# Performance work log

Hardware: AMD Instinct MI355X
Metric: run time of the kernel (lower is better)

The kernel has to match this reference:

```python
import jax, jax.numpy as jnp
import numpy as np

IN_F, OUT_F = 2048, 2048
N_EXPERTS, RANK, TOP_K = 8, 128, 2


def setup_inputs() -> dict:
    key = jax.random.key(0)
    k_x, k_r, k_a, k_b = jax.random.split(key, 4)
    hidden_states = jax.random.normal(k_x, (4, 4096, IN_F), dtype=jnp.float32)
    # router_proj.weight is [E, in]; we store it transposed so logits = x @ router_w
    router_w = jax.random.normal(k_r, (IN_F, N_EXPERTS), dtype=jnp.float32) * (IN_F ** -0.5)
    # expert e: a_proj [in, rank], b_proj [rank, out] (transposed nn.Linear weights)
    Wa = jax.random.normal(k_a, (N_EXPERTS, IN_F, RANK), dtype=jnp.float32) * (IN_F ** -0.5)
    Wb = jax.random.normal(k_b, (N_EXPERTS, RANK, OUT_F), dtype=jnp.float32) * (RANK ** -0.5)
    return {"hidden_states": hidden_states, "router_w": router_w, "Wa": Wa, "Wb": Wb}


def reference(hidden_states, router_w, Wa, Wb):
    B, S, D = hidden_states.shape
    x = hidden_states.reshape(-1, D)  # [T, in]
    # F.normalize(x, dim=-1): x / max(||x||_2, 1e-12)
    norm = jnp.maximum(jnp.linalg.norm(x, axis=-1, keepdims=True), 1e-12)
    router_logits = (x / norm) @ router_w  # [T, E]
    routing_weights = jax.nn.softmax(router_logits.astype(jnp.float32), axis=-1)
    rw, selected_experts = jax.lax.top_k(routing_weights, TOP_K)  # [T, k]
    rw = rw / jnp.sum(rw, axis=-1, keepdims=True)
    rw = rw.astype(hidden_states.dtype)
    # combine[t, e] = routing weight if expert e selected for token t, else 0.
    combine = jnp.sum(jax.nn.one_hot(selected_experts, N_EXPERTS, dtype=rw.dtype) * rw[..., None], axis=1)  # [T, E]
    out = jnp.zeros((x.shape[0], OUT_F), dtype=hidden_states.dtype)
    for e in range(N_EXPERTS):  # small fixed expert count
        out = out + combine[:, e, None] * ((x @ Wa[e]) @ Wb[e])
    return out.reshape(B, S, OUT_F)
```

## Files before the change

### kernel.cpp

```cpp
#include <hip/hip_runtime.h>
#include <cstdint>
#include <cstddef>

#define TOKENS 16384
#define DIM    2048
#define NEXP   8
#define RANK   128
#define NOUT   2048
#define CAP    8192
#define KSL    8

typedef __attribute__((ext_vector_type(4))) float    f32x4;
typedef __attribute__((ext_vector_type(8))) _Float16 f16x8;
typedef __attribute__((ext_vector_type(4))) _Float16 f16x4;

__device__ __forceinline__ void gload_lds16(const void* g, void* l) {
  __builtin_amdgcn_global_load_lds(
      (const __attribute__((address_space(1))) void*)g,
      (__attribute__((address_space(3))) void*)l, 16, 0, 0);
}

__global__ __launch_bounds__(256) void transpose_cast_f16(
    const float* __restrict__ in, _Float16* __restrict__ out,
    int R, int C, long ostride, long obase)
{
  __shared__ float tile[32][33];
  const int e = blockIdx.z;
  const float* ine = in + (size_t)e * R * C;
  const int c0 = blockIdx.x * 32, r0 = blockIdx.y * 32;
  const int tx = threadIdx.x, ty = threadIdx.y;
#pragma unroll
  for (int j = 0; j < 32; j += 8)
    tile[ty + j][tx] = ine[(size_t)(r0 + ty + j) * C + (c0 + tx)];
  __syncthreads();
#pragma unroll
  for (int j = 0; j < 32; j += 8)
    out[(size_t)e * obase + (size_t)(c0 + ty + j) * ostride + (r0 + tx)] =
        (_Float16)tile[tx][ty + j];
}

__global__ __launch_bounds__(256) void logits_fused_kernel(
    const float* __restrict__ x, const float* __restrict__ rw,
    float* __restrict__ lgpart, float* __restrict__ ssqpart,
    _Float16* __restrict__ xh)
{
  __shared__ __align__(16) char lds[16384];
  char* ldsBh = lds;
  char* ldsBe = lds + 8192;
  const int tid = threadIdx.x;
  const int w = tid >> 6, l = tid & 63;
  const int m0 = blockIdx.x * 128;
  const int ks = blockIdx.y;
  const int kbase = ks * 256;

#pragma unroll
  for (int i = 0; i < 16; ++i) {
    const int idx = tid * 16 + i;
    const int n = idx >> 8, k = idx & 255;
    const float v = (n < 8) ? rw[(size_t)(kbase + k) * 8 + n] : 0.f;
    const _Float16 h = (_Float16)v;
    const _Float16 e = (_Float16)(v - (float)h);
    const int off = n * 512 + ((k * 2) ^ ((n & 7) << 4));
    *(_Float16*)(ldsBh + off) = h;
    *(_Float16*)(ldsBe + off) = e;
  }
  __syncthreads();

  f32x4 acc[2];
  float ssl[2] = {0.f, 0.f};
#pragma unroll
  for (int mf = 0; mf < 2; ++mf)
#pragma unroll
    for (int j = 0; j < 4; ++j) acc[mf][j] = 0.f;

  for (int st = 0; st < 4; ++st) {
#pragma unroll
    for (int kk = 0; kk < 2; ++kk) {
      const int n = l & 15;
      const int bko = n * 512 +
          ((st * 128 + kk * 64 + ((l >> 4) << 4)) ^ ((n & 7) << 4));
      const f16x8 bh = *(const f16x8*)(ldsBh + bko);
      const f16x8 be = *(const f16x8*)(ldsBe + bko);
      const int c = kbase + st * 64 + kk * 32 + ((l >> 4) << 3);
#pragma unroll
      for (int mf = 0; mf < 2; ++mf) {
        const int r = m0 + w * 32 + mf * 16 + (l & 15);
        const float* xp = x + (size_t)r * DIM + c;
        const f32x4 va = *(const f32x4*)(xp);
        const f32x4 vb = *(const f32x4*)(xp + 4);
        float f[8] = {va[0], va[1], va[2], va[3], vb[0], vb[1], vb[2], vb[3]};
        f16x8 ah, ae;
#pragma unroll
        for (int j = 0; j < 8; ++j) {
          ah[j] = (_Float16)f[j];
          ae[j] = (_Float16)(f[j] - (float)ah[j]);
          ssl[mf] = fmaf(f[j], f[j], ssl[mf]);
        }
        *(f16x8*)(xh + (size_t)r * DIM + c) = ah;
        acc[mf] = __builtin_amdgcn_mfma_f32_16x16x32_f16(ae, bh, acc[mf], 0, 0, 0);
        acc[mf] = __builtin_amdgcn_mfma_f32_16x16x32_f16(ah, be, acc[mf], 0, 0, 0);
        acc[mf] = __builtin_amdgcn_mfma_f32_16x16x32_f16(ah, bh, acc[mf], 0, 0, 0);
      }
    }
  }

  const int col = l & 15;
  if (col < 8) {
#pragma unroll
    for (int mf = 0; mf < 2; ++mf) {
      const int rbase = m0 + w * 32 + mf * 16 + ((l >> 4) << 2);
#pragma unroll
      for (int j = 0; j < 4; ++j)
        lgpart[((size_t)ks * TOKENS + rbase + j) * 8 + col] = acc[mf][j];
    }
  }
#pragma unroll
  for (int mf = 0; mf < 2; ++mf) {
    float s = ssl[mf];
    s += __shfl_xor(s, 16, 64);
    s += __shfl_xor(s, 32, 64);
    if (l < 16)
      ssqpart[(size_t)ks * TOKENS + m0 + w * 32 + mf * 16 + l] = s;
  }
}

__global__ __launch_bounds__(256) void softmax_top2_kernel(
    const float* __restrict__ lgpart, const float* __restrict__ ssqpart,
    float* __restrict__ combine, int* __restrict__ pairinfo,
    int* __restrict__ counts, unsigned short* __restrict__ ids16)
{
  const size_t t = (size_t)blockIdx.x * 256 + threadIdx.x;
  float ss = 0.f;
  float lg[8];
#pragma unroll
  for (int e = 0; e < 8; ++e) lg[e] = 0.f;
#pragma unroll
  for (int ks = 0; ks < KSL; ++ks) {
    ss += ssqpart[(size_t)ks * TOKENS + t];
    const float* p = lgpart + ((size_t)ks * TOKENS + t) * 8;
    float4 a = *(const float4*)(p);
    float4 b = *(const float4*)(p + 4);
    lg[0] += a.x; lg[1] += a.y; lg[2] += a.z; lg[3] += a.w;
    lg[4] += b.x; lg[5] += b.y; lg[6] += b.z; lg[7] += b.w;
  }
  const float iv = 1.f / fmaxf(sqrtf(ss), 1e-12f);
#pragma unroll
  for (int e = 0; e < 8; ++e) lg[e] *= iv;
  float b1 = lg[0]; int e1 = 0;
#pragma unroll
  for (int e = 1; e < 8; ++e)
    if (lg[e] > b1) { b1 = lg[e]; e1 = e; }
  float b2 = -3.4e38f; int e2 = 0;
#pragma unroll
  for (int e = 0; e < 8; ++e)
    if (e != e1 && lg[e] > b2) { b2 = lg[e]; e2 = e; }
  const float p2 = expf(b2 - b1);
  const float w1 = 1.f / (1.f + p2);
  const float w2 = p2 * w1;
  float ov[8];
#pragma unroll
  for (int e = 0; e < 8; ++e)
    ov[e] = (e == e1) ? w1 : ((e == e2) ? w2 : 0.f);
  float4* cp = (float4*)(combine + t * 8);
  cp[0] = make_float4(ov[0], ov[1], ov[2], ov[3]);
  cp[1] = make_float4(ov[4], ov[5], ov[6], ov[7]);

  const int a = min(e1, e2), b = max(e1, e2);
  pairinfo[t] = a | (b << 8);
  const int bin = a * 8 + b;
  const int pos = atomicAdd(&counts[bin], 1);
  if (pos < CAP) ids16[bin * CAP + pos] = (unsigned short)t;
}

__global__ void make_items_kernel(const int* __restrict__ counts,
                                  int4* __restrict__ items)
{
  if (threadIdx.x == 0 && blockIdx.x == 0) {
    int j = 0;
    for (int b = 0; b < 64; ++b) {
      int c = counts[b]; if (c > CAP) c = CAP;
      for (int s = 0; s < c; s += 128)
        items[j++] = make_int4(b, b * CAP + s, min(128, c - s), 0);
    }
    for (; j < 192; ++j) items[j] = make_int4(-1, 0, 0, 0);
  }
}

__global__ __launch_bounds__(256) void gemm1_pair_kernel(
    const _Float16* __restrict__ xh, const _Float16* __restrict__ WaT,
    const float* __restrict__ combine, const unsigned short* __restrict__ ids,
    const int4* __restrict__ items, _Float16* __restrict__ Yc)
{
  __shared__ __align__(16) char lds[32768];
  __shared__ int ids_lds[128];
  char* ldsA = lds;
  char* ldsB = lds + 16384;
  const int4 item = items[blockIdx.y];
  if (item.x < 0) return;
  const int slot = blockIdx.x;
  const int e = slot ? (item.x & 7) : (item.x >> 3);
  const int tid = threadIdx.x;
  const int w = tid >> 6, l = tid & 63;
  const int wm = w >> 1, wn = w & 1;

  if (tid < 128)
    ids_lds[tid] = (tid < item.z) ? (int)ids[item.y + tid] : -1;
  __syncthreads();

  const int Lb = w * 1024 + l * 16;
  const _Float16* aptr[4];
  const _Float16* bptr[4];
  int ldst[4];
#pragma unroll
  for (int i = 0; i < 4; ++i) {
    const int L = i * 4096 + Lb;
    const int row = L >> 7;
    const int cb = (L & 127) ^ ((row & 7) << 4);
    int t = ids_lds[row]; if (t < 0) t = 0;
    aptr[i] = xh + (size_t)t * DIM + (cb >> 1);
    bptr[i] = WaT + (size_t)(e * 128 + row) * DIM + (cb >> 1);
    ldst[i] = i * 4096 + w * 1024;
  }

  f32x4 acc[4][4];
#pragma unroll
  for (int p = 0; p < 4; ++p)
#pragma unroll
    for (int q = 0; q < 4; ++q)
#pragma unroll
      for (int j = 0; j < 4; ++j) acc[p][q][j] = 0.f;

  for (int kt = 0; kt < DIM; kt += 64) {
#pragma unroll
    for (int i = 0; i < 4; ++i) {
      gload_lds16(aptr[i] + kt, ldsA + ldst[i]);
      gload_lds16(bptr[i] + kt, ldsB + ldst[i]);
    }
    __syncthreads();
#pragma unroll
    for (int kk = 0; kk < 2; ++kk) {
      const int kb = kk * 64 + ((l >> 4) << 4);
      f16x8 af[4], bfr[4];
#pragma unroll
      for (int mf = 0; mf < 4; ++mf) {
        const int r = (wm << 6) + (mf << 4) + (l & 15);
        af[mf] = *(const f16x8*)(ldsA + r * 128 + (kb ^ ((r & 7) << 4)));
      }
#pragma unroll
      for (int nf = 0; nf < 4; ++nf) {
        const int r = (wn << 6) + (nf << 4) + (l & 15);
        bfr[nf] = *(const f16x8*)(ldsB + r * 128 + (kb ^ ((r & 7) << 4)));
      }
#pragma unroll
      for (int mf = 0; mf < 4; ++mf)
#pragma unroll
        for (int nf = 0; nf < 4; ++nf)
          acc[mf][nf] = __builtin_amdgcn_mfma_f32_16x16x32_f16(
              af[mf], bfr[nf], acc[mf][nf], 0, 0, 0);
    }
    __syncthreads();
  }

  const int cr = (l >> 4) << 2;
  const int cc = l & 15;
#pragma unroll
  for (int mf = 0; mf < 4; ++mf) {
    const int lr0 = (wm << 6) + (mf << 4) + cr;
#pragma unroll
    for (int j = 0; j < 4; ++j) {
      const int t = ids_lds[lr0 + j];
      if (t < 0) continue;
      const float cs = combine[(size_t)t * 8 + e];
      _Float16* yr = Yc + (size_t)t * 256 + slot * 128;
#pragma unroll
      for (int nf = 0; nf < 4; ++nf)
        yr[(wn << 6) + (nf << 4) + cc] = (_Float16)(acc[mf][nf][j] * cs);
    }
  }
}

__global__ __launch_bounds__(256) void gemm2_pair_kernel(
    const _Float16* __restrict__ Y, const _Float16* __restrict__ WbT,
    const unsigned short* __restrict__ ids, const int4* __restrict__ items,
    float* __restrict__ out)
{
  __shared__ __align__(16) char lds[32768];
  __shared__ int ids_lds[128];
  char* ldsA = lds;
  char* ldsB = lds + 16384;
  const int4 item = items[blockIdx.y];
  if (item.x < 0) return;
  const int a = item.x >> 3, b = item.x & 7;
  const int n0 = blockIdx.x * 128;
  const int tid = threadIdx.x;
  const int w = tid >> 6, l = tid & 63;
  const int wm = w >> 1, wn = w & 1;

  if (tid < 128)
    ids_lds[tid] = (tid < item.z) ? (int)ids[item.y + tid] : -1;
  __syncthreads();

  const int Lb = w * 1024 + l * 16;
  const _Float16* aptr[4];
  const _Float16* bptrA[4];
  const _Float16* bptrB[4];
  int ldst[4];
#pragma unroll
  for (int i = 0; i < 4; ++i) {
    const int L = i * 4096 + Lb;
    const int row = L >> 7;
    const int cb = (L & 127) ^ ((row & 7) << 4);
    int t = ids_lds[row]; if (t < 0) t = 0;
    aptr[i]  = Y + (size_t)t * 256 + (cb >> 1);
    bptrA[i] = WbT + (size_t)(n0 + row) * 1024 + a * 128 + (cb >> 1);
    bptrB[i] = WbT + (size_t)(n0 + row) * 1024 + b * 128 + (cb >> 1);
    ldst[i] = i * 4096 + w * 1024;
  }

  f32x4 acc[4][4];
#pragma unroll
  for (int p = 0; p < 4; ++p)
#pragma unroll
    for (int q = 0; q < 4; ++q)
#pragma unroll
      for (int j = 0; j < 4; ++j) acc[p][q][j] = 0.f;

#pragma unroll
  for (int kt = 0; kt < 4; ++kt) {
#pragma unroll
    for (int i = 0; i < 4; ++i) {
      gload_lds16(aptr[i] + kt * 64, ldsA + ldst[i]);
      const _Float16* bs = (kt < 2) ? (bptrA[i] + kt * 64)
                                    : (bptrB[i] + (kt - 2) * 64);
      gload_lds16(bs, ldsB + ldst[i]);
    }
    __syncthreads();
#pragma unroll
    for (int kk = 0; kk < 2; ++kk) {
      const int kb = kk * 64 + ((l >> 4) << 4);
      f16x8 af[4], bfr[4];
#pragma unroll
      for (int mf = 0; mf < 4; ++mf) {
        const int r = (wm << 6) + (mf << 4) + (l & 15);
        af[mf] = *(const f16x8*)(ldsA + r * 128 + (kb ^ ((r & 7) << 4)));
      }
#pragma unroll
      for (int nf = 0; nf < 4; ++nf) {
        const int r = (wn << 6) + (nf << 4) + (l & 15);
        bfr[nf] = *(const f16x8*)(ldsB + r * 128 + (kb ^ ((r & 7) << 4)));
      }
#pragma unroll
      for (int mf = 0; mf < 4; ++mf)
#pragma unroll
        for (int nf = 0; nf < 4; ++nf)
          acc[mf][nf] = __builtin_amdgcn_mfma_f32_16x16x32_f16(
              af[mf], bfr[nf], acc[mf][nf], 0, 0, 0);
    }
    __syncthreads();
  }

  const int cr = (l >> 4) << 2;
  const int cc = l & 15;
#pragma unroll
  for (int mf = 0; mf < 4; ++mf) {
    const int lr0 = (wm << 6) + (mf << 4) + cr;
#pragma unroll
    for (int j = 0; j < 4; ++j) {
      const int t = ids_lds[lr0 + j];
      if (t < 0) continue;
      float* orow = out + (size_t)t * NOUT + n0;
#pragma unroll
      for (int nf = 0; nf < 4; ++nf)
        orow[(wn << 6) + (nf << 4) + cc] = acc[mf][nf][j];
    }
  }
}

extern "C" void kernel_launch(void* const* d_in, const int* in_sizes, int n_in,
                              void* d_out, int out_size, void* d_ws, size_t ws_size,
                              hipStream_t stream) {
  const float* x  = (const float*)d_in[0];
  const float* rw = (const float*)d_in[1];
  const float* Wa = (const float*)d_in[2];
  const float* Wb = (const float*)d_in[3];
  float* out = (float*)d_out;

  char* ws = (char*)d_ws;
  _Float16* xh       = (_Float16*)(ws);
  _Float16* WaT      = (_Float16*)(ws + 67108864);
  _Float16* WbT      = (_Float16*)(ws + 71303168);
  float*    combine  = (float*)   (ws + 75497472);
  int*      pairinfo = (int*)     (ws + 76021760);
  int*      counts   = (int*)     (ws + 76087296);
  int4*     items    = (int4*)    (ws + 76087552);
  unsigned short* ids16 = (unsigned short*)(ws + 76090624);
  _Float16* Yc       = (_Float16*)(ws + 77139200);
  float*    lgpart   = (float*)   (ws + 77139200);
  float*    ssqpart  = (float*)   (ws + 81333504);

  transpose_cast_f16<<<dim3(4, 64, 8), dim3(32, 8), 0, stream>>>(
      Wa, WaT, 2048, 128, 2048, (long)128 * 2048);
  transpose_cast_f16<<<dim3(64, 4, 8), dim3(32, 8), 0, stream>>>(
      Wb, WbT, 128, 2048, 1024, 128);

  logits_fused_kernel<<<dim3(TOKENS / 128, KSL), 256, 0, stream>>>(
      x, rw, lgpart, ssqpart, xh);

  hipMemsetAsync(counts, 0, 64 * sizeof(int), stream);
  softmax_top2_kernel<<<TOKENS / 256, 256, 0, stream>>>(
      lgpart, ssqpart, combine, pairinfo, counts, ids16);
  make_items_kernel<<<1, 64, 0, stream>>>(counts, items);

  gemm1_pair_kernel<<<dim3(2, 192), 256, 0, stream>>>(
      xh, WaT, combine, ids16, items, Yc);
  gemm2_pair_kernel<<<dim3(NOUT / 128, 192), 256, 0, stream>>>(
      Yc, WbT, ids16, items, out);
}
```

Measured before the change: 219.0 us.

## Fuse router logits and top-2 into one kernel; compute both experts per gemm1 block

Replaces the split-K MFMA logits kernel and the separate softmax/top-2 kernel with a single router kernel. Each wave handles one token row at a time, doing fp32 FMA dot products against an LDS-transposed router matrix and reducing with shuffles. This removes the partial-sum buffers and one launch, and it changes routing precision from split-fp16 MFMA to plain fp32. gemm1 now loads the A tile once and computes both paired experts in one block with a 256-wide N tile. That halves A traffic but doubles accumulator registers and raises LDS use to 48KB, which may reduce occupancy.

```diff
diff --git a/kernel.cpp b/kernel.cpp
--- a/kernel.cpp
+++ b/kernel.cpp
@@ -8,7 +8,6 @@
 #define RANK   128
 #define NOUT   2048
 #define CAP    8192
-#define KSL    8
 
 typedef __attribute__((ext_vector_type(4))) float    f32x4;
 typedef __attribute__((ext_vector_type(8))) _Float16 f16x8;
@@ -39,137 +38,92 @@
         (_Float16)tile[tx][ty + j];
 }
 
-__global__ __launch_bounds__(256) void logits_fused_kernel(
+__global__ __launch_bounds__(512) void router_kernel(
     const float* __restrict__ x, const float* __restrict__ rw,
-    float* __restrict__ lgpart, float* __restrict__ ssqpart,
-    _Float16* __restrict__ xh)
-{
-  __shared__ __align__(16) char lds[16384];
-  char* ldsBh = lds;
-  char* ldsBe = lds + 8192;
+    float* __restrict__ combine, int* __restrict__ counts,
+    unsigned short* __restrict__ ids16, _Float16* __restrict__ xh)
+{
+  __shared__ float rwT[NEXP][DIM];
   const int tid = threadIdx.x;
   const int w = tid >> 6, l = tid & 63;
-  const int m0 = blockIdx.x * 128;
-  const int ks = blockIdx.y;
-  const int kbase = ks * 256;
-
-#pragma unroll
-  for (int i = 0; i < 16; ++i) {
-    const int idx = tid * 16 + i;
-    const int n = idx >> 8, k = idx & 255;
-    const float v = (n < 8) ? rw[(size_t)(kbase + k) * 8 + n] : 0.f;
-    const _Float16 h = (_Float16)v;
-    const _Float16 e = (_Float16)(v - (float)h);
-    const int off = n * 512 + ((k * 2) ^ ((n & 7) << 4));
-    *(_Float16*)(ldsBh + off) = h;
-    *(_Float16*)(ldsBe + off) = e;
+
+  {
+    const int k0 = tid * 4;
+    f32x4 col[8];
+#pragma unroll
+    for (int j = 0; j < 4; ++j) {
+      const float4 lo = *(const float4*)(rw + (size_t)(k0 + j) * 8);
+      const float4 hi = *(const float4*)(rw + (size_t)(k0 + j) * 8 + 4);
+      col[0][j] = lo.x; col[1][j] = lo.y; col[2][j] = lo.z; col[3][j] = lo.w;
+      col[4][j] = hi.x; col[5][j] = hi.y; col[6][j] = hi.z; col[7][j] = hi.w;
+    }
+#pragma unroll
+    for (int e = 0; e < 8; ++e)
+      *(f32x4*)&rwT[e][k0] = col[e];
   }
   __syncthreads();
 
-  f32x4 acc[2];
-  float ssl[2] = {0.f, 0.f};
-#pragma unroll
-  for (int mf = 0; mf < 2; ++mf)
-#pragma unroll
-    for (int j = 0; j < 4; ++j) acc[mf][j] = 0.f;
-
-  for (int st = 0; st < 4; ++st) {
-#pragma unroll
-    for (int kk = 0; kk < 2; ++kk) {
-      const int n = l & 15;
-      const int bko = n * 512 +
-          ((st * 128 + kk * 64 + ((l >> 4) << 4)) ^ ((n & 7) << 4));
-      const f16x8 bh = *(const f16x8*)(ldsBh + bko);
-      const f16x8 be = *(const f16x8*)(ldsBe + bko);
-      const int c = kbase + st * 64 + kk * 32 + ((l >> 4) << 3);
-#pragma unroll
-      for (int mf = 0; mf < 2; ++mf) {
-        const int r = m0 + w * 32 + mf * 16 + (l & 15);
-        const float* xp = x + (size_t)r * DIM + c;
-        const f32x4 va = *(const f32x4*)(xp);
-        const f32x4 vb = *(const f32x4*)(xp + 4);
-        float f[8] = {va[0], va[1], va[2], va[3], vb[0], vb[1], vb[2], vb[3]};
-        f16x8 ah, ae;
-#pragma unroll
-        for (int j = 0; j < 8; ++j) {
-          ah[j] = (_Float16)f[j];
-          ae[j] = (_Float16)(f[j] - (float)ah[j]);
-          ssl[mf] = fmaf(f[j], f[j], ssl[mf]);
-        }
-        *(f16x8*)(xh + (size_t)r * DIM + c) = ah;
-        acc[mf] = __builtin_amdgcn_mfma_f32_16x16x32_f16(ae, bh, acc[mf], 0, 0, 0);
-        acc[mf] = __builtin_amdgcn_mfma_f32_16x16x32_f16(ah, be, acc[mf], 0, 0, 0);
-        acc[mf] = __builtin_amdgcn_mfma_f32_16x16x32_f16(ah, bh, acc[mf], 0, 0, 0);
-      }
-    }
-  }
-
-  const int col = l & 15;
-  if (col < 8) {
-#pragma unroll
-    for (int mf = 0; mf < 2; ++mf) {
-      const int rbase = m0 + w * 32 + mf * 16 + ((l >> 4) << 2);
-#pragma unroll
-      for (int j = 0; j < 4; ++j)
-        lgpart[((size_t)ks * TOKENS + rbase + j) * 8 + col] = acc[mf][j];
-    }
-  }
-#pragma unroll
-  for (int mf = 0; mf < 2; ++mf) {
-    float s = ssl[mf];
-    s += __shfl_xor(s, 16, 64);
-    s += __shfl_xor(s, 32, 64);
-    if (l < 16)
-      ssqpart[(size_t)ks * TOKENS + m0 + w * 32 + mf * 16 + l] = s;
-  }
-}
-
-__global__ __launch_bounds__(256) void softmax_top2_kernel(
-    const float* __restrict__ lgpart, const float* __restrict__ ssqpart,
-    float* __restrict__ combine, int* __restrict__ pairinfo,
-    int* __restrict__ counts, unsigned short* __restrict__ ids16)
-{
-  const size_t t = (size_t)blockIdx.x * 256 + threadIdx.x;
-  float ss = 0.f;
-  float lg[8];
-#pragma unroll
-  for (int e = 0; e < 8; ++e) lg[e] = 0.f;
-#pragma unroll
-  for (int ks = 0; ks < KSL; ++ks) {
-    ss += ssqpart[(size_t)ks * TOKENS + t];
-    const float* p = lgpart + ((size_t)ks * TOKENS + t) * 8;
-    float4 a = *(const float4*)(p);
-    float4 b = *(const float4*)(p + 4);
-    lg[0] += a.x; lg[1] += a.y; lg[2] += a.z; lg[3] += a.w;
-    lg[4] += b.x; lg[5] += b.y; lg[6] += b.z; lg[7] += b.w;
-  }
-  const float iv = 1.f / fmaxf(sqrtf(ss), 1e-12f);
-#pragma unroll
-  for (int e = 0; e < 8; ++e) lg[e] *= iv;
-  float b1 = lg[0]; int e1 = 0;
-#pragma unroll
-  for (int e = 1; e < 8; ++e)
-    if (lg[e] > b1) { b1 = lg[e]; e1 = e; }
-  float b2 = -3.4e38f; int e2 = 0;
-#pragma unroll
-  for (int e = 0; e < 8; ++e)
-    if (e != e1 && lg[e] > b2) { b2 = lg[e]; e2 = e; }
-  const float p2 = expf(b2 - b1);
-  const float w1 = 1.f / (1.f + p2);
-  const float w2 = p2 * w1;
-  float ov[8];
-#pragma unroll
-  for (int e = 0; e < 8; ++e)
-    ov[e] = (e == e1) ? w1 : ((e == e2) ? w2 : 0.f);
-  float4* cp = (float4*)(combine + t * 8);
-  cp[0] = make_float4(ov[0], ov[1], ov[2], ov[3]);
-  cp[1] = make_float4(ov[4], ov[5], ov[6], ov[7]);
-
-  const int a = min(e1, e2), b = max(e1, e2);
-  pairinfo[t] = a | (b << 8);
-  const int bin = a * 8 + b;
-  const int pos = atomicAdd(&counts[bin], 1);
-  if (pos < CAP) ids16[bin * CAP + pos] = (unsigned short)t;
+  for (int i = 0; i < 4; ++i) {
+    const size_t t = (size_t)blockIdx.x * 32 + w * 4 + i;
+    const float* xr  = x  + t * DIM;
+    _Float16*    xhr = xh + t * DIM;
+
+    float ss = 0.f;
+    float lg[8];
+#pragma unroll
+    for (int e = 0; e < 8; ++e) lg[e] = 0.f;
+
+#pragma unroll
+    for (int j = 0; j < 8; ++j) {
+      const int k = j * 256 + l * 4;
+      const float4 v = *(const float4*)(xr + k);
+      f16x4 hv;
+      hv.x = (_Float16)v.x; hv.y = (_Float16)v.y;
+      hv.z = (_Float16)v.z; hv.w = (_Float16)v.w;
+      *(f16x4*)(xhr + k) = hv;
+      ss = fmaf(v.x, v.x, fmaf(v.y, v.y, fmaf(v.z, v.z, fmaf(v.w, v.w, ss))));
+#pragma unroll
+      for (int e = 0; e < 8; ++e) {
+        const f32x4 rv = *(const f32x4*)&rwT[e][k];
+        lg[e] = fmaf(v.x, rv[0],
+                fmaf(v.y, rv[1], fmaf(v.z, rv[2], fmaf(v.w, rv[3], lg[e]))));
+      }
+    }
+#pragma unroll
+    for (int m = 1; m < 64; m <<= 1) {
+      ss += __shfl_xor(ss, m, 64);
+#pragma unroll
+      for (int e = 0; e < 8; ++e) lg[e] += __shfl_xor(lg[e], m, 64);
+    }
+    if (l == 0) {
+      const float iv = 1.f / fmaxf(sqrtf(ss), 1e-12f);
+#pragma unroll
+      for (int e = 0; e < 8; ++e) lg[e] *= iv;
+      float b1 = lg[0]; int e1 = 0;
+#pragma unroll
+      for (int e = 1; e < 8; ++e)
+        if (lg[e] > b1) { b1 = lg[e]; e1 = e; }
+      float b2 = -3.4e38f; int e2 = 0;
+#pragma unroll
+      for (int e = 0; e < 8; ++e)
+        if (e != e1 && lg[e] > b2) { b2 = lg[e]; e2 = e; }
+      const float p2 = expf(b2 - b1);
+      const float w1 = 1.f / (1.f + p2);
+      const float w2 = p2 * w1;
+      float ov[8];
+#pragma unroll
+      for (int e = 0; e < 8; ++e)
+        ov[e] = (e == e1) ? w1 : ((e == e2) ? w2 : 0.f);
+      float4* cp = (float4*)(combine + t * 8);
+      cp[0] = make_float4(ov[0], ov[1], ov[2], ov[3]);
+      cp[1] = make_float4(ov[4], ov[5], ov[6], ov[7]);
+
+      const int a = min(e1, e2), b = max(e1, e2);
+      const int bin = a * 8 + b;
+      const int pos = atomicAdd(&counts[bin], 1);
+      if (pos < CAP) ids16[bin * CAP + pos] = (unsigned short)t;
+    }
+  }
 }
 
 __global__ void make_items_kernel(const int* __restrict__ counts,
@@ -191,14 +145,13 @@
     const float* __restrict__ combine, const unsigned short* __restrict__ ids,
     const int4* __restrict__ items, _Float16* __restrict__ Yc)
 {
-  __shared__ __align__(16) char lds[32768];
+  __shared__ __align__(16) char lds[49152];
   __shared__ int ids_lds[128];
   char* ldsA = lds;
   char* ldsB = lds + 16384;
-  const int4 item = items[blockIdx.y];
+  const int4 item = items[blockIdx.x];
   if (item.x < 0) return;
-  const int slot = blockIdx.x;
-  const int e = slot ? (item.x & 7) : (item.x >> 3);
+  const int ea = item.x >> 3, eb = item.x & 7;
   const int tid = threadIdx.x;
   const int w = tid >> 6, l = tid & 63;
   const int wm = w >> 1, wn = w & 1;
@@ -209,8 +162,8 @@
 
   const int Lb = w * 1024 + l * 16;
   const _Float16* aptr[4];
-  const _Float16* bptr[4];
-  int ldst[4];
+  const _Float16* bptr[8];
+  int ldstA[4], ldstB[8];
 #pragma unroll
   for (int i = 0; i < 4; ++i) {
     const int L = i * 4096 + Lb;
@@ -218,49 +171,59 @@
     const int cb = (L & 127) ^ ((row & 7) << 4);
     int t = ids_lds[row]; if (t < 0) t = 0;
     aptr[i] = xh + (size_t)t * DIM + (cb >> 1);
-    bptr[i] = WaT + (size_t)(e * 128 + row) * DIM + (cb >> 1);
-    ldst[i] = i * 4096 + w * 1024;
-  }
-
-  f32x4 acc[4][4];
+    ldstA[i] = i * 4096 + w * 1024;
+  }
+#pragma unroll
+  for (int i = 0; i < 8; ++i) {
+    const int L = i * 4096 + Lb;
+    const int row = L >> 7;
+    const int cb = (L & 127) ^ ((row & 7) << 4);
+    const int e = (row < 128) ? ea : eb;
+    bptr[i] = WaT + (size_t)(e * 128 + (row & 127)) * DIM + (cb >> 1);
+    ldstB[i] = i * 4096 + w * 1024;
+  }
+
+  f32x4 acc[4][8];
 #pragma unroll
   for (int p = 0; p < 4; ++p)
 #pragma unroll
-    for (int q = 0; q < 4; ++q)
+    for (int q = 0; q < 8; ++q)
 #pragma unroll
       for (int j = 0; j < 4; ++j) acc[p][q][j] = 0.f;
 
   for (int kt = 0; kt < DIM; kt += 64) {
 #pragma unroll
-    for (int i = 0; i < 4; ++i) {
-      gload_lds16(aptr[i] + kt, ldsA + ldst[i]);
-      gload_lds16(bptr[i] + kt, ldsB + ldst[i]);
-    }
+    for (int i = 0; i < 4; ++i)
+      gload_lds16(aptr[i] + kt, ldsA + ldstA[i]);
+#pragma unroll
+    for (int i = 0; i < 8; ++i)
+      gload_lds16(bptr[i] + kt, ldsB + ldstB[i]);
     __syncthreads();
 #pragma unroll
     for (int kk = 0; kk < 2; ++kk) {
       const int kb = kk * 64 + ((l >> 4) << 4);
-      f16x8 af[4], bfr[4];
+      f16x8 af[4], bfr[8];
 #pragma unroll
       for (int mf = 0; mf < 4; ++mf) {
         const int r = (wm << 6) + (mf << 4) + (l & 15);
         af[mf] = *(const f16x8*)(ldsA + r * 128 + (kb ^ ((r & 7) << 4)));
       }
 #pragma unroll
-      for (int nf = 0; nf < 4; ++nf) {
-        const int r = (wn << 6) + (nf << 4) + (l & 15);
+      for (int nf = 0; nf < 8; ++nf) {
+        const int r = (wn << 7) + (nf << 4) + (l & 15);
         bfr[nf] = *(const f16x8*)(ldsB + r * 128 + (kb ^ ((r & 7) << 4)));
       }
 #pragma unroll
       for (int mf = 0; mf < 4; ++mf)
 #pragma unroll
-        for (int nf = 0; nf < 4; ++nf)
+        for (int nf = 0; nf < 8; ++nf)
           acc[mf][nf] = __builtin_amdgcn_mfma_f32_16x16x32_f16(
               af[mf], bfr[nf], acc[mf][nf], 0, 0, 0);
     }
     __syncthreads();
   }
 
+  const int e_sel = wn ? eb : ea;
   const int cr = (l >> 4) << 2;
   const int cc = l & 15;
 #pragma unroll
@@ -270,11 +233,11 @@
     for (int j = 0; j < 4; ++j) {
       const int t = ids_lds[lr0 + j];
       if (t < 0) continue;
-      const float cs = combine[(size_t)t * 8 + e];
-      _Float16* yr = Yc + (size_t)t * 256 + slot * 128;
-#pragma unroll
-      for (int nf = 0; nf < 4; ++nf)
-        yr[(wn << 6) + (nf << 4) + cc] = (_Float16)(acc[mf][nf][j] * cs);
+      const float cs = combine[(size_t)t * 8 + e_sel];
+      _Float16* yr = Yc + (size_t)t * 256 + wn * 128;
+#pragma unroll
+      for (int nf = 0; nf < 8; ++nf)
+        yr[(nf << 4) + cc] = (_Float16)(acc[mf][nf][j] * cs);
     }
   }
 }
@@ -386,32 +349,26 @@
   float* out = (float*)d_out;
 
   char* ws = (char*)d_ws;
-  _Float16* xh       = (_Float16*)(ws);
-  _Float16* WaT      = (_Float16*)(ws + 67108864);
-  _Float16* WbT      = (_Float16*)(ws + 71303168);
-  float*    combine  = (float*)   (ws + 75497472);
-  int*      pairinfo = (int*)     (ws + 76021760);
-  int*      counts   = (int*)     (ws + 76087296);
-  int4*     items    = (int4*)    (ws + 76087552);
-  unsigned short* ids16 = (unsigned short*)(ws + 76090624);
-  _Float16* Yc       = (_Float16*)(ws + 77139200);
-  float*    lgpart   = (float*)   (ws + 77139200);
-  float*    ssqpart  = (float*)   (ws + 81333504);
+  _Float16* xh      = (_Float16*)(ws);
+  _Float16* WaT     = (_Float16*)(ws + 67108864);
+  _Float16* WbT     = (_Float16*)(ws + 71303168);
+  float*    combine = (float*)   (ws + 75497472);
+  int*      counts  = (int*)     (ws + 76021760);
+  int4*     items   = (int4*)    (ws + 76022016);
+  unsigned short* ids16 = (unsigned short*)(ws + 76025088);
+  _Float16* Yc      = (_Float16*)(ws + 77073664);
 
   transpose_cast_f16<<<dim3(4, 64, 8), dim3(32, 8), 0, stream>>>(
       Wa, WaT, 2048, 128, 2048, (long)128 * 2048);
   transpose_cast_f16<<<dim3(64, 4, 8), dim3(32, 8), 0, stream>>>(
       Wb, WbT, 128, 2048, 1024, 128);
 
-  logits_fused_kernel<<<dim3(TOKENS / 128, KSL), 256, 0, stream>>>(
-      x, rw, lgpart, ssqpart, xh);
-
   hipMemsetAsync(counts, 0, 64 * sizeof(int), stream);
-  softmax_top2_kernel<<<TOKENS / 256, 256, 0, stream>>>(
-      lgpart, ssqpart, combine, pairinfo, counts, ids16);
+  router_kernel<<<TOKENS / 32, 512, 0, stream>>>(
+      x, rw, combine, counts, ids16, xh);
   make_items_kernel<<<1, 64, 0, stream>>>(counts, items);
 
-  gemm1_pair_kernel<<<dim3(2, 192), 256, 0, stream>>>(
+  gemm1_pair_kernel<<<192, 256, 0, stream>>>(
       xh, WaT, combine, ids16, items, Yc);
   gemm2_pair_kernel<<<dim3(NOUT / 128, 192), 256, 0, stream>>>(
       Yc, WbT, ids16, items, out);
```

New measurement: 278.0 us. 27.0% more time.
